# Performance work log

Hardware: AMD Instinct MI355X
Metric: run time of the kernel (lower is better)

## Reference

```python
import jax, jax.numpy as jnp
import numpy as np

B, S, D, H = 8, 1024, 768, 12
C = D // H  # head dim = 64
NEG_SLOPE = 0.2  # PyG GATConv default leaky_relu slope


def setup_inputs() -> dict:
    key = jax.random.key(0)
    ks = jax.random.split(key, 12)
    s = 0.02
    return {
        "hidden_states": jax.random.normal(ks[0], (B, S, D), jnp.float32),
        "transformer_output": jax.random.normal(ks[1], (B, S, D), jnp.float32),
        # GATConv params: lin (no bias), att_src/att_dst [H, C], bias [H*C]
        "W_gat": jax.random.normal(ks[2], (D, D), jnp.float32) * s,
        "att_src": jax.random.normal(ks[3], (H, C), jnp.float32) * s,
        "att_dst": jax.random.normal(ks[4], (H, C), jnp.float32) * s,
        "b_gat": jnp.zeros((D,), jnp.float32),
        # gat_projection
        "W_proj": jax.random.normal(ks[5], (D, D), jnp.float32) * s,
        "b_proj": jnp.zeros((D,), jnp.float32),
        # fusion
        "W_fus": jax.random.normal(ks[6], (2 * D, D), jnp.float32) * s,
        "b_fus": jnp.zeros((D,), jnp.float32),
    }


def reference(hidden_states, transformer_output, W_gat, att_src, att_dst,
              b_gat, W_proj, b_proj, W_fus, b_fus):
    # --- GATConv on a fully-connected graph (+ default self-loops) ---
    # Fully connected + self loops => softmax over ALL sources per target,
    # so the scatter-softmax reduces to dense attention.
    x = (hidden_states @ W_gat).reshape(B, S, H, C)          # [B,S,H,C]
    a_src = jnp.einsum('bshc,hc->bhs', x, att_src)           # score contribution of source j
    a_dst = jnp.einsum('bshc,hc->bhs', x, att_dst)           # score contribution of target i
    # scores[b,h,i,j] = a_dst_i + a_src_j, then leaky_relu, softmax over j
    scores = jax.nn.leaky_relu(a_dst[:, :, :, None] + a_src[:, :, None, :],
                               negative_slope=NEG_SLOPE)     # [B,H,S,S]
    attn = jax.nn.softmax(scores, axis=-1)
    out = jnp.einsum('bhij,bjhc->bihc', attn, x)             # aggregate sources
    gat_out = out.reshape(B, S, D) + b_gat                   # concat heads + bias

    # --- projection, fusion ---
    graph_output = gat_out @ W_proj + b_proj
    fused = jnp.concatenate([transformer_output, graph_output], axis=-1)
    fused = fused @ W_fus + b_fus
    return fused
```

## Files before the change

### kernel.cpp

```cpp
#include <hip/hip_runtime.h>
#include <hip/hip_bf16.h>

#define NB 8
#define NS 1024
#define ND 768
#define NH 12
#define NC 64
#define NEG 0.2f
#define NBUK 128

typedef __attribute__((ext_vector_type(8))) short bf16x8;
typedef __attribute__((ext_vector_type(4))) float f32x4;

static __device__ __forceinline__ float bf2f(unsigned short u) {
    union { float f; unsigned int i; } v; v.i = ((unsigned int)u) << 16; return v.f;
}
static __device__ __forceinline__ unsigned short f2bf(float f) {
    union { float f; unsigned int i; } v; v.f = f;
    unsigned int r = v.i + 0x7FFFu + ((v.i >> 16) & 1u);
    return (unsigned short)(r >> 16);
}

static __device__ __forceinline__ void gload16(const unsigned short* g, unsigned short* l) {
    __builtin_amdgcn_global_load_lds((const __attribute__((address_space(1))) void*)g,
                                     (__attribute__((address_space(3))) void*)l, 16, 0, 0);
}

static __device__ __forceinline__ int swz_bid(int orig, int nwg) {
    int q = nwg >> 3, r = nwg & 7;
    int xcd = orig & 7, idx = orig >> 3;
    return (xcd < r ? xcd * (q + 1) : r * (q + 1) + (xcd - r) * q) + idx;
}

__global__ __launch_bounds__(256) void k_prep(const float* __restrict__ hs, const float* __restrict__ to,
                                              const float* __restrict__ Wp, const float* __restrict__ Wg,
                                              const float* __restrict__ Wf, const float* __restrict__ bp,
                                              const float* __restrict__ bfu,
                                              unsigned short* __restrict__ h_bf, unsigned short* __restrict__ t_bf,
                                              unsigned short* __restrict__ Wp_bf, unsigned short* __restrict__ WgT,
                                              unsigned short* __restrict__ WfT, float* __restrict__ bias_tot,
                                              int n1, int n2) {
    const int NT1 = (ND / 32) * (3 * ND / 32);
    const int NT2 = (ND * 8) / 256;
    int blk = blockIdx.x, t = threadIdx.x;
    if (blk < NT1) {
        __shared__ float tile[32][33];
        int bx = blk % (ND / 32), by = blk / (ND / 32);
        const float* src; unsigned short* dst; int K, k0;
        if (by < ND / 32) { src = Wg; dst = WgT; K = ND; k0 = by * 32; }
        else { src = Wf; dst = WfT; K = 2 * ND; k0 = (by - ND / 32) * 32; }
        int n0 = bx * 32;
        int r = t >> 3, c4 = (t & 7) * 4;
        float4 v = *reinterpret_cast<const float4*>(src + (size_t)(k0 + r) * ND + n0 + c4);
        tile[r][c4] = v.x; tile[r][c4 + 1] = v.y; tile[r][c4 + 2] = v.z; tile[r][c4 + 3] = v.w;
        __syncthreads();
        ushort4 o;
        o.x = f2bf(tile[c4][r]); o.y = f2bf(tile[c4 + 1][r]);
        o.z = f2bf(tile[c4 + 2][r]); o.w = f2bf(tile[c4 + 3][r]);
        *reinterpret_cast<ushort4*>(dst + (size_t)(n0 + r) * K + k0 + c4) = o;
    } else if (blk < NT1 + NT2) {
        int gid = (blk - NT1) * 256 + t;
        int c = gid >> 3, sl = gid & 7;
        float acc = 0.f;
        int k0 = sl * 96;
#pragma unroll 8
        for (int k = k0; k < k0 + 96; k++) acc += bp[k] * Wf[(size_t)(ND + k) * ND + c];
        acc += __shfl_down(acc, 1, 64);
        acc += __shfl_down(acc, 2, 64);
        acc += __shfl_down(acc, 4, 64);
        if (sl == 0) bias_tot[c] = acc + bfu[c];
    } else {
        int gid = (blk - NT1 - NT2) * 256 + t;
        const float* s; unsigned short* d; int i;
        if (gid < n1) { s = hs; d = h_bf; i = gid; }
        else if (gid < 2 * n1) { s = to; d = t_bf; i = gid - n1; }
        else { s = Wp; d = Wp_bf; i = gid - 2 * n1; if (i >= n2) return; }
        i *= 4;
        float4 v = *reinterpret_cast<const float4*>(s + i);
        ushort4 o;
        o.x = f2bf(v.x); o.y = f2bf(v.y); o.z = f2bf(v.z); o.w = f2bf(v.w);
        *reinterpret_cast<ushort4*>(d + i) = o;
    }
}

__global__ __launch_bounds__(256) void k_bucket(const float* __restrict__ a_src,
                                                float4* __restrict__ pack,
                                                int* __restrict__ bstart,
                                                float* __restrict__ smax_g,
                                                float2* __restrict__ bparam,
                                                float* __restrict__ zb) {
    int bh = blockIdx.x, t = threadIdx.x;
    __shared__ float v[1024];
    __shared__ int bi[1024];
    __shared__ float red[256];
    __shared__ int cnt[NBUK], pre[NBUK];
    __shared__ float zs1[NBUK], zs2[NBUK];
    for (int i = t; i < 1024; i += 256) v[i] = a_src[(size_t)bh * 1024 + i];
    if (t < NBUK) { cnt[t] = 0; zs1[t] = 0.f; zs2[t] = 0.f; }
    __syncthreads();
    float lm = -1e30f, ln = 1e30f;
    for (int i = t; i < 1024; i += 256) { lm = fmaxf(lm, v[i]); ln = fminf(ln, v[i]); }
    red[t] = lm; __syncthreads();
    for (int s = 128; s > 0; s >>= 1) { if (t < s) red[t] = fmaxf(red[t], red[t + s]); __syncthreads(); }
    float mx = red[0]; __syncthreads();
    red[t] = ln; __syncthreads();
    for (int s = 128; s > 0; s >>= 1) { if (t < s) red[t] = fminf(red[t], red[t + s]); __syncthreads(); }
    float mn = red[0]; __syncthreads();
    float scale = (float)NBUK / fmaxf(mx - mn, 1e-20f);
    for (int i = t; i < 1024; i += 256) {
        int bk = (int)((v[i] - mn) * scale);
        bk = min(max(bk, 0), NBUK - 1);
        bi[i] = bk;
        atomicAdd(&cnt[bk], 1);
    }
    __syncthreads();
    if (t < NBUK) pre[t] = cnt[t];
    __syncthreads();
    for (int off = 1; off < NBUK; off <<= 1) {
        int x = (t >= off && t < NBUK) ? pre[t - off] : 0;
        __syncthreads();
        if (t < NBUK) pre[t] += x;
        __syncthreads();
    }
    if (t < NBUK) {
        int start = pre[t] - cnt[t];
        bstart[bh * (NBUK + 1) + t] = start;
        cnt[t] = start;
    }
    if (t == 0) {
        bstart[bh * (NBUK + 1) + NBUK] = 1024;
        smax_g[bh] = mx;
        bparam[bh] = make_float2(mn, scale);
    }
    __syncthreads();
    for (int i = t; i < 1024; i += 256) {
        int pos = atomicAdd(&cnt[bi[i]], 1);
        float u = v[i] - mx;
        float4 p;
        p.x = u; p.y = __expf(u); p.z = __expf(0.2f * u); p.w = __int_as_float(i);
        pack[(size_t)bh * 1024 + pos] = p;
        atomicAdd(&zs1[bi[i]], p.y);
        atomicAdd(&zs2[bi[i]], p.z);
    }
    __syncthreads();
    for (int off = 1; off < NBUK; off <<= 1) {
        float x1 = (t >= off && t < NBUK) ? zs1[t - off] : 0.f;
        float x2 = (t >= off && t < NBUK) ? zs2[t - off] : 0.f;
        __syncthreads();
        if (t < NBUK) { zs1[t] += x1; zs2[t] += x2; }
        __syncthreads();
    }
    if (t < NBUK) {
        zb[(size_t)(bh * NBUK + t) * 2] = zs1[t];
        zb[(size_t)(bh * NBUK + t) * 2 + 1] = zs2[t];
    }
}

__global__ __launch_bounds__(256) void k_bsum(const unsigned short* __restrict__ x_bf,
                                              const float4* __restrict__ pack,
                                              const int* __restrict__ bstart,
                                              float* __restrict__ P) {
    int grp = blockIdx.x, bh = blockIdx.y;
    int t = threadIdx.x, w = t >> 6, lane = t & 63;
    int b = bh / NH, h = bh % NH;
    const float4* pk = pack + (size_t)bh * 1024;
    const unsigned short* xb = x_bf + (size_t)b * NS * ND + h * 64 + lane;
#pragma unroll
    for (int r = 0; r < 2; r++) {
        int bk = grp * 8 + w * 2 + r;
        int ks = bstart[bh * (NBUK + 1) + bk], ke = bstart[bh * (NBUK + 1) + bk + 1];
        float V1 = 0.f, V2 = 0.f;
        for (int k = ks; k < ke; k++) {
            float4 p = pk[k];
            int j = __float_as_int(p.w);
            float xv = bf2f(xb[(size_t)j * ND]);
            V1 += p.y * xv; V2 += p.z * xv;
        }
        size_t o = ((size_t)(bh * NBUK + bk) * 2) * 64 + lane;
        P[o] = V1; P[o + 64] = V2;
    }
}

__global__ __launch_bounds__(256) void k_bpref(float* __restrict__ P) {
    int bh = blockIdx.x, t = threadIdx.x, w = t >> 6, lane = t & 63;
    __shared__ float segV[4][2][64];
    size_t base = (size_t)bh * NBUK;
    float V1 = 0.f, V2 = 0.f;
    for (int g = 0; g < 4; ++g) {
        float a1[8], a2[8];
#pragma unroll
        for (int r = 0; r < 8; r++) {
            size_t o = ((base + w * 32 + g * 8 + r) * 2) * 64 + lane;
            a1[r] = P[o]; a2[r] = P[o + 64];
        }
#pragma unroll
        for (int r = 0; r < 8; r++) { V1 += a1[r]; a1[r] = V1; V2 += a2[r]; a2[r] = V2; }
#pragma unroll
        for (int r = 0; r < 8; r++) {
            size_t o = ((base + w * 32 + g * 8 + r) * 2) * 64 + lane;
            P[o] = a1[r]; P[o + 64] = a2[r];
        }
    }
    segV[w][0][lane] = V1; segV[w][1][lane] = V2;
    __syncthreads();
    if (w > 0) {
        float O1 = 0.f, O2 = 0.f;
        for (int w2 = 0; w2 < w; w2++) { O1 += segV[w2][0][lane]; O2 += segV[w2][1][lane]; }
        for (int g = 0; g < 4; ++g) {
            float a1[8], a2[8];
#pragma unroll
            for (int r = 0; r < 8; r++) {
                size_t o = ((base + w * 32 + g * 8 + r) * 2) * 64 + lane;
                a1[r] = P[o]; a2[r] = P[o + 64];
            }
#pragma unroll
            for (int r = 0; r < 8; r++) {
                size_t o = ((base + w * 32 + g * 8 + r) * 2) * 64 + lane;
                P[o] = a1[r] + O1; P[o + 64] = a2[r] + O2;
            }
        }
    }
}

__global__ __launch_bounds__(256) void k_apply3(const float* __restrict__ P,
                                                const float* __restrict__ zb,
                                                const float* __restrict__ a_dst,
                                                const float* __restrict__ smax_g,
                                                const float2* __restrict__ bparam,
                                                const float* __restrict__ b_gat,
                                                unsigned short* __restrict__ gat) {
    int bh = blockIdx.y, t = threadIdx.x, w = t >> 6, lane = t & 63;
    int b = bh / NH, h = bh % NH;
    float sm = smax_g[bh];
    float2 bp_ = bparam[bh];
    float mn = bp_.x, scale = bp_.y;
    size_t pb = (size_t)bh * NBUK;
    float T1 = P[((pb + NBUK - 1) * 2) * 64 + lane];
    float z1tot = zb[(pb + NBUK - 1) * 2];
    float bias = b_gat[h * 64 + lane];
#pragma unroll
    for (int q = 0; q < 8; q++) {
        int i = blockIdx.x * 32 + w * 8 + q;
        float d = a_dst[(size_t)bh * 1024 + i];
        float dm = d + sm;
        float m = dm > 0.f ? dm : NEG * dm;
        float c1 = __expf(dm - m);
        float c2 = __expf(NEG * dm - m);
        int e = (int)floorf((-d - mn) * scale + 0.5f);
        e = min(max(e, 0), NBUK);
        float P1f = 0.f, P2f = 0.f, z1f = 0.f, z2f = 0.f;
        if (e > 0) {
            size_t o = ((pb + e - 1) * 2) * 64 + lane;
            P1f = P[o]; P2f = P[o + 64];
            z1f = zb[(pb + e - 1) * 2];
            z2f = zb[(pb + e - 1) * 2 + 1];
        }
        float num = c1 * (T1 - P1f) + c2 * P2f;
        float Z = c1 * (z1tot - z1f) + c2 * z2f;
        gat[((size_t)(b * NS + i)) * ND + h * 64 + lane] = f2bf(num / Z + bias);
    }
}

template <bool OUT_BF16, bool BIAS, bool DUAL, bool ATT>
static __device__ __forceinline__ void gemm_body(
    const unsigned short* __restrict__ A1, const unsigned short* __restrict__ B1,
    int lda1, int ldb1,
    const unsigned short* __restrict__ A2, const unsigned short* __restrict__ B2,
    int lda2, int ldb2,
    const float* __restrict__ bias, void* __restrict__ Cout,
    int m0, int n0, int N, int K,
    unsigned short* sA, unsigned short* sB,
    const float* __restrict__ att_src, const float* __restrict__ att_dst,
    float* __restrict__ a_src, float* __restrict__ a_dst) {
    int t = threadIdx.x, wave = t >> 6, lane = t & 63;
    int lr = lane & 15, kq = lane >> 4;
    int srow = t >> 3;
    int scol = ((t & 7) ^ (srow & 7)) * 8;
    int cs0 = ((kq) ^ (lr & 7)) * 8;
    int cs1 = ((4 + kq) ^ (lr & 7)) * 8;
    const int kh = K >> 6;
    const int nsteps = (DUAL ? 2 : 1) * kh;
    f32x4 acc[4][2] = {};

    auto STAGE = [&](int s, int buf) {
        const unsigned short* A; const unsigned short* Bt; int lda, ldb, k0;
        if (DUAL && s >= kh) { A = A2; Bt = B2; lda = lda2; ldb = ldb2; k0 = (s - kh) << 6; }
        else { A = A1; Bt = B1; lda = lda1; ldb = ldb1; k0 = s << 6; }
        const unsigned short* gA = A + (size_t)(m0 + srow) * lda + scol + k0;
        const unsigned short* gB = Bt + (size_t)(n0 + srow) * ldb + scol + k0;
        unsigned short* dA = sA + buf * 4096 + t * 8;
        unsigned short* dB = sB + buf * 8192 + t * 8;
        gload16(gA, dA);
        gload16(gA + (size_t)32 * lda, dA + 2048);
        gload16(gB, dB);
        gload16(gB + (size_t)32 * ldb, dB + 2048);
        gload16(gB + (size_t)64 * ldb, dB + 4096);
        gload16(gB + (size_t)96 * ldb, dB + 6144);
    };

    STAGE(0, 0);
    __syncthreads();
    for (int s = 0; s < nsteps; s++) {
        int cur = s & 1;
        if (s + 1 < nsteps) STAGE(s + 1, cur ^ 1);
        unsigned short* cA = sA + cur * 4096;
        unsigned short* cB = sB + cur * 8192;
        bf16x8 a0[4], a1v[4], b0[2], b1v[2];
#pragma unroll
        for (int m = 0; m < 4; m++) {
            a0[m]  = *reinterpret_cast<bf16x8*>(&cA[(m * 16 + lr) * 64 + cs0]);
            a1v[m] = *reinterpret_cast<bf16x8*>(&cA[(m * 16 + lr) * 64 + cs1]);
        }
#pragma unroll
        for (int n = 0; n < 2; n++) {
            b0[n]  = *reinterpret_cast<bf16x8*>(&cB[(wave * 32 + n * 16 + lr) * 64 + cs0]);
            b1v[n] = *reinterpret_cast<bf16x8*>(&cB[(wave * 32 + n * 16 + lr) * 64 + cs1]);
        }
#pragma unroll
        for (int m = 0; m < 4; m++)
#pragma unroll
            for (int n = 0; n < 2; n++) {
                acc[m][n] = __builtin_amdgcn_mfma_f32_16x16x32_bf16(a0[m], b0[n], acc[m][n], 0, 0, 0);
                acc[m][n] = __builtin_amdgcn_mfma_f32_16x16x32_bf16(a1v[m], b1v[n], acc[m][n], 0, 0, 0);
            }
        __syncthreads();
    }

    int rg = kq * 4;
#pragma unroll
    for (int m = 0; m < 4; m++) {
#pragma unroll
        for (int n = 0; n < 2; n++) {
            int col = n0 + wave * 32 + n * 16 + lr;
            float bv = BIAS ? bias[col] : 0.0f;
#pragma unroll
            for (int r = 0; r < 4; r++) {
                int row = m0 + m * 16 + rg + r;
                float v = acc[m][n][r] + bv;
                if (OUT_BF16) {
                    ((unsigned short*)Cout)[(size_t)row * N + col] = f2bf(v);
                } else {
                    ((float*)Cout)[(size_t)row * N + col] = v;
                }
            }
        }
    }

    if (ATT) {
        float ds_[4][4] = {}, dd_[4][4] = {};
#pragma unroll
        for (int n = 0; n < 2; n++) {
            int colg = n0 + wave * 32 + n * 16 + lr;
            float as_v = att_src[colg];
            float ad_v = att_dst[colg];
#pragma unroll
            for (int m = 0; m < 4; m++)
#pragma unroll
                for (int r = 0; r < 4; r++) {
                    ds_[m][r] = fmaf(acc[m][n][r], as_v, ds_[m][r]);
                    dd_[m][r] = fmaf(acc[m][n][r], ad_v, dd_[m][r]);
                }
        }
#pragma unroll
        for (int off = 1; off <= 8; off <<= 1)
#pragma unroll
            for (int m = 0; m < 4; m++)
#pragma unroll
                for (int r = 0; r < 4; r++) {
                    ds_[m][r] += __shfl_xor(ds_[m][r], off, 64);
                    dd_[m][r] += __shfl_xor(dd_[m][r], off, 64);
                }
        float* red = (float*)sA;
        if (lr == 0) {
#pragma unroll
            for (int m = 0; m < 4; m++)
#pragma unroll
                for (int r = 0; r < 4; r++) {
                    int rl = m * 16 + kq * 4 + r;
                    red[wave * 64 + rl] = ds_[m][r];
                    red[256 + wave * 64 + rl] = dd_[m][r];
                }
        }
        __syncthreads();
        if (t < 128) {
            int hb = t >> 6, rl = t & 63;
            float vs = red[(hb * 2) * 64 + rl] + red[(hb * 2 + 1) * 64 + rl];
            float vd = red[256 + (hb * 2) * 64 + rl] + red[256 + (hb * 2 + 1) * 64 + rl];
            int grow = m0 + rl;
            int b = grow >> 10, sdx = grow & 1023;
            int head = (n0 >> 6) + hb;
            a_src[((size_t)b * NH + head) * NS + sdx] = vs;
            a_dst[((size_t)b * NH + head) * NS + sdx] = vd;
        }
    }
}

__global__ __launch_bounds__(256) void k_gemm_pair(
    const unsigned short* __restrict__ Aa, const unsigned short* __restrict__ Ba,
    unsigned short* __restrict__ Ca, int NBna, int Na, int Ka, int lda_a, int ldb_a, int nwg_a,
    const unsigned short* __restrict__ Ab, const unsigned short* __restrict__ Bb,
    unsigned short* __restrict__ Cb, int NBnb, int Nb, int Kb, int lda_b, int ldb_b,
    const float* __restrict__ att_src, const float* __restrict__ att_dst,
    float* __restrict__ a_src, float* __restrict__ a_dst) {
    __shared__ alignas(16) unsigned short sA[2 * 64 * 64];
    __shared__ alignas(16) unsigned short sB[2 * 128 * 64];
    int wg = swz_bid(blockIdx.x, gridDim.x);
    if (wg < nwg_a) {
        gemm_body<true, false, false, true>(Aa, Ba, lda_a, ldb_a, nullptr, nullptr, 0, 0, nullptr,
                                            Ca, (wg / NBna) * 64, (wg % NBna) * 128, Na, Ka, sA, sB,
                                            att_src, att_dst, a_src, a_dst);
    } else {
        wg -= nwg_a;
        gemm_body<true, false, false, false>(Ab, Bb, lda_b, ldb_b, nullptr, nullptr, 0, 0, nullptr,
                                             Cb, (wg / NBnb) * 64, (wg % NBnb) * 128, Nb, Kb, sA, sB,
                                             nullptr, nullptr, nullptr, nullptr);
    }
}

__global__ __launch_bounds__(256) void k_gemm_dual(
    const unsigned short* __restrict__ A1, const unsigned short* __restrict__ B1,
    const unsigned short* __restrict__ A2, const unsigned short* __restrict__ B2,
    const float* __restrict__ bias, float* __restrict__ out,
    int NBn, int N, int K, int lda, int ldb1, int ldb2) {
    __shared__ alignas(16) unsigned short sA[2 * 64 * 64];
    __shared__ alignas(16) unsigned short sB[2 * 128 * 64];
    int wg = swz_bid(blockIdx.x, gridDim.x);
    gemm_body<false, true, true, false>(A1, B1, lda, ldb1, A2, B2, lda, ldb2, bias,
                                        out, (wg / NBn) * 64, (wg % NBn) * 128, N, K, sA, sB,
                                        nullptr, nullptr, nullptr, nullptr);
}

extern "C" void kernel_launch(void* const* d_in, const int* in_sizes, int n_in,
                              void* d_out, int out_size, void* d_ws, size_t ws_size,
                              hipStream_t stream) {
    const float* hs  = (const float*)d_in[0];
    const float* to  = (const float*)d_in[1];
    const float* Wg  = (const float*)d_in[2];
    const float* asv = (const float*)d_in[3];
    const float* adv = (const float*)d_in[4];
    const float* bg  = (const float*)d_in[5];
    const float* Wp  = (const float*)d_in[6];
    const float* bp  = (const float*)d_in[7];
    const float* Wf  = (const float*)d_in[8];
    const float* bfu = (const float*)d_in[9];
    float* out = (float*)d_out;

    char* ws = (char*)d_ws;
    size_t off = 0;
    auto alloc = [&](size_t bytes) -> void* {
        void* p = ws + off;
        off = (off + bytes + 255) & ~(size_t)255;
        return p;
    };
    const size_t NBSD = (size_t)NB * NS * ND;
    const int NBH = NB * NH;
    unsigned short* h_bf   = (unsigned short*)alloc(NBSD * 2);
    unsigned short* x_bf   = (unsigned short*)alloc(NBSD * 2);
    unsigned short* t_bf   = (unsigned short*)alloc(NBSD * 2);
    unsigned short* WgT    = (unsigned short*)alloc((size_t)ND * ND * 2);
    unsigned short* Wp_bf  = (unsigned short*)alloc((size_t)ND * ND * 2);
    unsigned short* WfT    = (unsigned short*)alloc((size_t)2 * ND * ND * 2);
    unsigned short* WcombT = (unsigned short*)alloc((size_t)ND * ND * 2);
    float*  bias_tot = (float*)alloc((size_t)ND * 4);
    float*  a_src = (float*)alloc((size_t)NBH * NS * 4);
    float*  a_dst = (float*)alloc((size_t)NBH * NS * 4);
    float4* pack  = (float4*)alloc((size_t)NBH * NS * 16);
    int*    bstart = (int*)alloc((size_t)NBH * (NBUK + 1) * 4);
    float*  P     = (float*)alloc((size_t)NBH * NBUK * 2 * 64 * 4);
    float*  zb    = (float*)alloc((size_t)NBH * NBUK * 2 * 4);
    float*  smaxb = (float*)alloc((size_t)NBH * 4);
    float2* bparam = (float2*)alloc((size_t)NBH * 8);

    int n1 = (int)NBSD / 4, n2 = ND * ND / 4;
    const int NT1 = (ND / 32) * (3 * ND / 32);
    const int NT2 = (ND * 8) / 256;
    const int NT3 = (2 * n1 + n2 + 255) / 256;
    k_prep<<<NT1 + NT2 + NT3, 256, 0, stream>>>(hs, to, Wp, Wg, Wf, bp, bfu,
                                                h_bf, t_bf, Wp_bf, WgT, WfT, bias_tot, n1, n2);

    int nwg1 = (NB * NS / 64) * (ND / 128);
    int nwgW = (ND / 64) * (ND / 128);
    k_gemm_pair<<<nwg1 + nwgW, 256, 0, stream>>>(
        h_bf, WgT, x_bf, ND / 128, ND, ND, ND, ND, nwg1,
        WfT + ND, Wp_bf, WcombT, ND / 128, ND, ND, 2 * ND, ND,
        asv, adv, a_src, a_dst);

    k_bucket<<<NBH, 256, 0, stream>>>(a_src, pack, bstart, smaxb, bparam, zb);
    k_bsum<<<dim3(NBUK / 8, NBH), 256, 0, stream>>>(x_bf, pack, bstart, P);
    k_bpref<<<NBH, 256, 0, stream>>>(P);

    unsigned short* gat_bf = h_bf;
    k_apply3<<<dim3(NS / 32, NBH), 256, 0, stream>>>(P, zb, a_dst, smaxb, bparam, bg, gat_bf);

    k_gemm_dual<<<(NB * NS / 64) * (ND / 128), 256, 0, stream>>>(
        t_bf, WfT, gat_bf, WcombT, bias_tot, out, ND / 128, ND, ND, ND, 2 * ND, ND);
}
```

Baseline: 137.1 us.

## Load GEMM A tiles straight from global into registers, bypassing LDS

The A operand no longer goes through shared memory. Each wave loads its A fragments from global memory directly into MFMA register layout, double-buffered across two register sets while B stays staged in LDS. This removes the A LDS writes and reads and shrinks LDS use, which may raise occupancy. The cost is that all four waves now load the same A rows redundantly from global/L2, the A loads are less coalesced, and register pressure goes up.

Result: slower. 216.9 us (+58.2%).

```diff
diff --git a/kernel.cpp b/kernel.cpp
--- a/kernel.cpp
+++ b/kernel.cpp
@@ -269,7 +269,7 @@
     int lda2, int ldb2,
     const float* __restrict__ bias, void* __restrict__ Cout,
     int m0, int n0, int N, int K,
-    unsigned short* sA, unsigned short* sB,
+    unsigned short* sB,
     const float* __restrict__ att_src, const float* __restrict__ att_dst,
     float* __restrict__ a_src, float* __restrict__ a_dst) {
     int t = threadIdx.x, wave = t >> 6, lane = t & 63;
@@ -282,35 +282,31 @@
     const int nsteps = (DUAL ? 2 : 1) * kh;
     f32x4 acc[4][2] = {};
 
-    auto STAGE = [&](int s, int buf) {
-        const unsigned short* A; const unsigned short* Bt; int lda, ldb, k0;
-        if (DUAL && s >= kh) { A = A2; Bt = B2; lda = lda2; ldb = ldb2; k0 = (s - kh) << 6; }
-        else { A = A1; Bt = B1; lda = lda1; ldb = ldb1; k0 = s << 6; }
-        const unsigned short* gA = A + (size_t)(m0 + srow) * lda + scol + k0;
+    auto STAGE_B = [&](int s, int buf) {
+        const unsigned short* Bt; int ldb, k0;
+        if (DUAL && s >= kh) { Bt = B2; ldb = ldb2; k0 = (s - kh) << 6; }
+        else { Bt = B1; ldb = ldb1; k0 = s << 6; }
         const unsigned short* gB = Bt + (size_t)(n0 + srow) * ldb + scol + k0;
-        unsigned short* dA = sA + buf * 4096 + t * 8;
         unsigned short* dB = sB + buf * 8192 + t * 8;
-        gload16(gA, dA);
-        gload16(gA + (size_t)32 * lda, dA + 2048);
         gload16(gB, dB);
         gload16(gB + (size_t)32 * ldb, dB + 2048);
         gload16(gB + (size_t)64 * ldb, dB + 4096);
         gload16(gB + (size_t)96 * ldb, dB + 6144);
     };
-
-    STAGE(0, 0);
-    __syncthreads();
-    for (int s = 0; s < nsteps; s++) {
-        int cur = s & 1;
-        if (s + 1 < nsteps) STAGE(s + 1, cur ^ 1);
-        unsigned short* cA = sA + cur * 4096;
-        unsigned short* cB = sB + cur * 8192;
-        bf16x8 a0[4], a1v[4], b0[2], b1v[2];
-#pragma unroll
-        for (int m = 0; m < 4; m++) {
-            a0[m]  = *reinterpret_cast<bf16x8*>(&cA[(m * 16 + lr) * 64 + cs0]);
-            a1v[m] = *reinterpret_cast<bf16x8*>(&cA[(m * 16 + lr) * 64 + cs1]);
-        }
+    auto LOADA = [&](int s, bf16x8 (&ar)[4][2]) {
+        const unsigned short* A; int lda, k0;
+        if (DUAL && s >= kh) { A = A2; lda = lda2; k0 = (s - kh) << 6; }
+        else { A = A1; lda = lda1; k0 = s << 6; }
+        const unsigned short* gA = A + (size_t)(m0 + lr) * lda + k0 + kq * 8;
+#pragma unroll
+        for (int m = 0; m < 4; m++)
+#pragma unroll
+            for (int kk = 0; kk < 2; kk++)
+                ar[m][kk] = *reinterpret_cast<const bf16x8*>(gA + (size_t)(m * 16) * lda + kk * 32);
+    };
+    auto COMPUTE = [&](int buf, bf16x8 (&ar)[4][2]) {
+        unsigned short* cB = sB + buf * 8192;
+        bf16x8 b0[2], b1v[2];
 #pragma unroll
         for (int n = 0; n < 2; n++) {
             b0[n]  = *reinterpret_cast<bf16x8*>(&cB[(wave * 32 + n * 16 + lr) * 64 + cs0]);
@@ -320,9 +316,21 @@
         for (int m = 0; m < 4; m++)
 #pragma unroll
             for (int n = 0; n < 2; n++) {
-                acc[m][n] = __builtin_amdgcn_mfma_f32_16x16x32_bf16(a0[m], b0[n], acc[m][n], 0, 0, 0);
-                acc[m][n] = __builtin_amdgcn_mfma_f32_16x16x32_bf16(a1v[m], b1v[n], acc[m][n], 0, 0, 0);
+                acc[m][n] = __builtin_amdgcn_mfma_f32_16x16x32_bf16(ar[m][0], b0[n], acc[m][n], 0, 0, 0);
+                acc[m][n] = __builtin_amdgcn_mfma_f32_16x16x32_bf16(ar[m][1], b1v[n], acc[m][n], 0, 0, 0);
             }
+    };
+
+    bf16x8 A0r[4][2], A1r[4][2];
+    STAGE_B(0, 0);
+    LOADA(0, A0r);
+    __syncthreads();
+    for (int s = 0; s < nsteps; s += 2) {
+        if (s + 1 < nsteps) { STAGE_B(s + 1, 1); LOADA(s + 1, A1r); }
+        COMPUTE(0, A0r);
+        __syncthreads();
+        if (s + 2 < nsteps) { STAGE_B(s + 2, 0); LOADA(s + 2, A0r); }
+        if (s + 1 < nsteps) COMPUTE(1, A1r);
         __syncthreads();
     }
 
@@ -370,7 +378,7 @@
                     ds_[m][r] += __shfl_xor(ds_[m][r], off, 64);
                     dd_[m][r] += __shfl_xor(dd_[m][r], off, 64);
                 }
-        float* red = (float*)sA;
+        float* red = (float*)sB;
         if (lr == 0) {
 #pragma unroll
             for (int m = 0; m < 4; m++)
@@ -402,17 +410,16 @@
     unsigned short* __restrict__ Cb, int NBnb, int Nb, int Kb, int lda_b, int ldb_b,
     const float* __restrict__ att_src, const float* __restrict__ att_dst,
     float* __restrict__ a_src, float* __restrict__ a_dst) {
-    __shared__ alignas(16) unsigned short sA[2 * 64 * 64];
     __shared__ alignas(16) unsigned short sB[2 * 128 * 64];
     int wg = swz_bid(blockIdx.x, gridDim.x);
     if (wg < nwg_a) {
         gemm_body<true, false, false, true>(Aa, Ba, lda_a, ldb_a, nullptr, nullptr, 0, 0, nullptr,
-                                            Ca, (wg / NBna) * 64, (wg % NBna) * 128, Na, Ka, sA, sB,
+                                            Ca, (wg / NBna) * 64, (wg % NBna) * 128, Na, Ka, sB,
                                             att_src, att_dst, a_src, a_dst);
     } else {
         wg -= nwg_a;
         gemm_body<true, false, false, false>(Ab, Bb, lda_b, ldb_b, nullptr, nullptr, 0, 0, nullptr,
-                                             Cb, (wg / NBnb) * 64, (wg % NBnb) * 128, Nb, Kb, sA, sB,
+                                             Cb, (wg / NBnb) * 64, (wg % NBnb) * 128, Nb, Kb, sB,
                                              nullptr, nullptr, nullptr, nullptr);
     }
 }
@@ -422,11 +429,10 @@
     const unsigned short* __restrict__ A2, const unsigned short* __restrict__ B2,
     const float* __restrict__ bias, float* __restrict__ out,
     int NBn, int N, int K, int lda, int ldb1, int ldb2) {
-    __shared__ alignas(16) unsigned short sA[2 * 64 * 64];
     __shared__ alignas(16) unsigned short sB[2 * 128 * 64];
     int wg = swz_bid(blockIdx.x, gridDim.x);
     gemm_body<false, true, true, false>(A1, B1, lda, ldb1, A2, B2, lda, ldb2, bias,
-                                        out, (wg / NBn) * 64, (wg % NBn) * 128, N, K, sA, sB,
+                                        out, (wg / NBn) * 64, (wg % NBn) * 128, N, K, sB,
                                         nullptr, nullptr, nullptr, nullptr);
 }
 
```

## Split fusion GEMM: compute transformer half early, accumulate graph half later

Applied to the files above, without the earlier changes.

The final dual-K GEMM is split in two. The transformer_output @ W_fus_top half (plus bias) now runs as a third group of workgroups inside the first combined GEMM launch, writing fp32 straight into the output. The last kernel then only runs the K=768 GEMM on the GAT output and adds its result into the existing output via read-modify-write. This takes half of the critical-path work off the tail and fills the first launch with more independent blocks, at the cost of an extra fp32 read of the output in the last kernel.

New measurement: 144.8 us. 1.06x slower.

```diff
diff --git a/kernel.cpp b/kernel.cpp
--- a/kernel.cpp
+++ b/kernel.cpp
@@ -261,12 +261,10 @@
     }
 }
 
-template <bool OUT_BF16, bool BIAS, bool DUAL, bool ATT>
+template <bool OUT_BF16, bool BIAS, bool ACC, bool ATT>
 static __device__ __forceinline__ void gemm_body(
-    const unsigned short* __restrict__ A1, const unsigned short* __restrict__ B1,
-    int lda1, int ldb1,
-    const unsigned short* __restrict__ A2, const unsigned short* __restrict__ B2,
-    int lda2, int ldb2,
+    const unsigned short* __restrict__ A, const unsigned short* __restrict__ Bt,
+    int lda, int ldb,
     const float* __restrict__ bias, void* __restrict__ Cout,
     int m0, int n0, int N, int K,
     unsigned short* sA, unsigned short* sB,
@@ -278,24 +276,21 @@
     int scol = ((t & 7) ^ (srow & 7)) * 8;
     int cs0 = ((kq) ^ (lr & 7)) * 8;
     int cs1 = ((4 + kq) ^ (lr & 7)) * 8;
-    const int kh = K >> 6;
-    const int nsteps = (DUAL ? 2 : 1) * kh;
+    const int nsteps = K >> 6;
     f32x4 acc[4][2] = {};
+    const unsigned short* gA = A + (size_t)(m0 + srow) * lda + scol;
+    const unsigned short* gB = Bt + (size_t)(n0 + srow) * ldb + scol;
 
     auto STAGE = [&](int s, int buf) {
-        const unsigned short* A; const unsigned short* Bt; int lda, ldb, k0;
-        if (DUAL && s >= kh) { A = A2; Bt = B2; lda = lda2; ldb = ldb2; k0 = (s - kh) << 6; }
-        else { A = A1; Bt = B1; lda = lda1; ldb = ldb1; k0 = s << 6; }
-        const unsigned short* gA = A + (size_t)(m0 + srow) * lda + scol + k0;
-        const unsigned short* gB = Bt + (size_t)(n0 + srow) * ldb + scol + k0;
+        int k0 = s << 6;
         unsigned short* dA = sA + buf * 4096 + t * 8;
         unsigned short* dB = sB + buf * 8192 + t * 8;
-        gload16(gA, dA);
-        gload16(gA + (size_t)32 * lda, dA + 2048);
-        gload16(gB, dB);
-        gload16(gB + (size_t)32 * ldb, dB + 2048);
-        gload16(gB + (size_t)64 * ldb, dB + 4096);
-        gload16(gB + (size_t)96 * ldb, dB + 6144);
+        gload16(gA + k0, dA);
+        gload16(gA + (size_t)32 * lda + k0, dA + 2048);
+        gload16(gB + k0, dB);
+        gload16(gB + (size_t)32 * ldb + k0, dB + 2048);
+        gload16(gB + (size_t)64 * ldb + k0, dB + 4096);
+        gload16(gB + (size_t)96 * ldb + k0, dB + 6144);
     };
 
     STAGE(0, 0);
@@ -340,7 +335,9 @@
                 if (OUT_BF16) {
                     ((unsigned short*)Cout)[(size_t)row * N + col] = f2bf(v);
                 } else {
-                    ((float*)Cout)[(size_t)row * N + col] = v;
+                    float* o = (float*)Cout + (size_t)row * N + col;
+                    if (ACC) v += *o;
+                    *o = v;
                 }
             }
         }
@@ -395,39 +392,46 @@
     }
 }
 
-__global__ __launch_bounds__(256) void k_gemm_pair(
-    const unsigned short* __restrict__ Aa, const unsigned short* __restrict__ Ba,
-    unsigned short* __restrict__ Ca, int NBna, int Na, int Ka, int lda_a, int ldb_a, int nwg_a,
-    const unsigned short* __restrict__ Ab, const unsigned short* __restrict__ Bb,
-    unsigned short* __restrict__ Cb, int NBnb, int Nb, int Kb, int lda_b, int ldb_b,
+__global__ __launch_bounds__(256) void k_gemm_tri(
+    const unsigned short* __restrict__ A1, const unsigned short* __restrict__ B1,
+    unsigned short* __restrict__ C1, int nwg1,
+    const unsigned short* __restrict__ A2, const unsigned short* __restrict__ B2,
+    unsigned short* __restrict__ C2, int nwg2,
+    const unsigned short* __restrict__ A3, const unsigned short* __restrict__ B3,
+    float* __restrict__ C3, const float* __restrict__ bias,
     const float* __restrict__ att_src, const float* __restrict__ att_dst,
     float* __restrict__ a_src, float* __restrict__ a_dst) {
     __shared__ alignas(16) unsigned short sA[2 * 64 * 64];
     __shared__ alignas(16) unsigned short sB[2 * 128 * 64];
+    const int NBn = ND / 128;
     int wg = swz_bid(blockIdx.x, gridDim.x);
-    if (wg < nwg_a) {
-        gemm_body<true, false, false, true>(Aa, Ba, lda_a, ldb_a, nullptr, nullptr, 0, 0, nullptr,
-                                            Ca, (wg / NBna) * 64, (wg % NBna) * 128, Na, Ka, sA, sB,
+    if (wg < nwg1) {
+        gemm_body<true, false, false, true>(A1, B1, ND, ND, nullptr, C1,
+                                            (wg / NBn) * 64, (wg % NBn) * 128, ND, ND, sA, sB,
                                             att_src, att_dst, a_src, a_dst);
+    } else if (wg < nwg1 + nwg2) {
+        wg -= nwg1;
+        gemm_body<true, false, false, false>(A2, B2, 2 * ND, ND, nullptr, C2,
+                                             (wg / NBn) * 64, (wg % NBn) * 128, ND, ND, sA, sB,
+                                             nullptr, nullptr, nullptr, nullptr);
     } else {
-        wg -= nwg_a;
-        gemm_body<true, false, false, false>(Ab, Bb, lda_b, ldb_b, nullptr, nullptr, 0, 0, nullptr,
-                                             Cb, (wg / NBnb) * 64, (wg % NBnb) * 128, Nb, Kb, sA, sB,
+        wg -= nwg1 + nwg2;
+        gemm_body<false, true, false, false>(A3, B3, ND, 2 * ND, bias, C3,
+                                             (wg / NBn) * 64, (wg % NBn) * 128, ND, ND, sA, sB,
                                              nullptr, nullptr, nullptr, nullptr);
     }
 }
 
-__global__ __launch_bounds__(256) void k_gemm_dual(
-    const unsigned short* __restrict__ A1, const unsigned short* __restrict__ B1,
-    const unsigned short* __restrict__ A2, const unsigned short* __restrict__ B2,
-    const float* __restrict__ bias, float* __restrict__ out,
-    int NBn, int N, int K, int lda, int ldb1, int ldb2) {
+__global__ __launch_bounds__(256) void k_gemm_acc(
+    const unsigned short* __restrict__ A, const unsigned short* __restrict__ B,
+    float* __restrict__ out) {
     __shared__ alignas(16) unsigned short sA[2 * 64 * 64];
     __shared__ alignas(16) unsigned short sB[2 * 128 * 64];
+    const int NBn = ND / 128;
     int wg = swz_bid(blockIdx.x, gridDim.x);
-    gemm_body<false, true, true, false>(A1, B1, lda, ldb1, A2, B2, lda, ldb2, bias,
-                                        out, (wg / NBn) * 64, (wg % NBn) * 128, N, K, sA, sB,
-                                        nullptr, nullptr, nullptr, nullptr);
+    gemm_body<false, false, true, false>(A, B, ND, ND, nullptr, out,
+                                         (wg / NBn) * 64, (wg % NBn) * 128, ND, ND, sA, sB,
+                                         nullptr, nullptr, nullptr, nullptr);
 }
 
 extern "C" void kernel_launch(void* const* d_in, const int* in_sizes, int n_in,
@@ -480,9 +484,11 @@
 
     int nwg1 = (NB * NS / 64) * (ND / 128);
     int nwgW = (ND / 64) * (ND / 128);
-    k_gemm_pair<<<nwg1 + nwgW, 256, 0, stream>>>(
-        h_bf, WgT, x_bf, ND / 128, ND, ND, ND, ND, nwg1,
-        WfT + ND, Wp_bf, WcombT, ND / 128, ND, ND, 2 * ND, ND,
+    int nwg3 = (NB * NS / 64) * (ND / 128);
+    k_gemm_tri<<<nwg1 + nwgW + nwg3, 256, 0, stream>>>(
+        h_bf, WgT, x_bf, nwg1,
+        WfT + ND, Wp_bf, WcombT, nwgW,
+        t_bf, WfT, out, bias_tot,
         asv, adv, a_src, a_dst);
 
     k_bucket<<<NBH, 256, 0, stream>>>(a_src, pack, bstart, smaxb, bparam, zb);
@@ -492,6 +498,5 @@
     unsigned short* gat_bf = h_bf;
     k_apply3<<<dim3(NS / 32, NBH), 256, 0, stream>>>(P, zb, a_dst, smaxb, bparam, bg, gat_bf);
 
-    k_gemm_dual<<<(NB * NS / 64) * (ND / 128), 256, 0, stream>>>(
-        t_bf, WfT, gat_bf, WcombT, bias_tot, out, ND / 128, ND, ND, ND, 2 * ND, ND);
-}
+    k_gemm_acc<<<(NB * NS / 64) * (ND / 128), 256, 0, stream>>>(gat_bf, WcombT, out);
+}
```
